# Optimization experiments

Measured on AMD Instinct MI355X. Metric: run time of the kernel, lower is better.

## Reference

```python
import jax, jax.numpy as jnp
import numpy as np
import math

CHUNK = 128  # hardcoded chunk_size in the original module


def setup_inputs() -> dict:
    key = jax.random.key(0)
    ks = jax.random.split(key, 6)
    B, C, T, H, W = 8, 256, 16, 8, 8
    KC, VC = 8192, 512  # key_channels, value_channels (dk = KC/heads = T*H*W = 1024)
    return {
        "x": jax.random.normal(ks[0], (B, C, T, H, W), dtype=jnp.float32),
        "Wk": jax.random.normal(ks[1], (KC, C), dtype=jnp.float32) * 0.02,
        "Wq": jax.random.normal(ks[2], (KC, C), dtype=jnp.float32) * 0.02,
        "Wv": jax.random.normal(ks[3], (VC, C), dtype=jnp.float32) * 0.02,
        "Wr": jax.random.normal(ks[4], (C, VC), dtype=jnp.float32) * 0.02,
        "br": jnp.zeros((C,), dtype=jnp.float32),
        "num_heads": 8,
    }


def reference(x, Wk, Wq, Wv, Wr, br, num_heads):
    B, C, T, H, W = x.shape
    N = T * H * W
    # 1x1x1 Conv3d == per-position linear projection
    k = jnp.einsum('oc,bcthw->bothw', Wk, x).reshape(B, num_heads, -1, N)
    q = jnp.einsum('oc,bcthw->bothw', Wq, x).reshape(B, num_heads, -1, N)
    v = jnp.einsum('oc,bcthw->bothw', Wv, x).reshape(B, num_heads, -1, N)
    dk = k.shape[2]  # == N by structural constraint of the original matmul
    # matmul(keys, q_chunk) over all chunks at once (matmul is linear in q):
    # contracts keys' position axis with queries' channel axis, as in torch.
    scores = jnp.matmul(k, q) / math.sqrt(dk)  # [B, h, dk, N]
    # softmax applied per query-chunk of size CHUNK along the last axis
    nchunks = N // CHUNK
    attn = jax.nn.softmax(
        scores.reshape(B, num_heads, dk, nchunks, CHUNK), axis=-1
    ).reshape(B, num_heads, dk, N)
    out = jnp.matmul(v, attn)  # [B, h, dv, N] (dk == N)
    out = out.reshape(B, -1, T, H, W)
    out = jnp.einsum('oc,bcthw->bothw', Wr, out) + br[None, :, None, None, None]
    return out
```

## Files before the change

### kernel.cpp

```cpp
#include <hip/hip_runtime.h>
#include <hip/hip_bf16.h>


using bf16x8 = __attribute__((ext_vector_type(8))) __bf16;
using f32x4  = __attribute__((ext_vector_type(4))) float;
using s16x4  = __attribute__((ext_vector_type(4))) short;

static __device__ __forceinline__ short f2b(float f) {
  union { float f; unsigned u; } v; v.f = f;
  unsigned r = v.u + 0x7fffu + ((v.u >> 16) & 1u);
  return (short)(r >> 16);
}

static __device__ __forceinline__ void gll16(const void* g, void* l) {
  __builtin_amdgcn_global_load_lds(
      (const __attribute__((address_space(1))) void*)g,
      (__attribute__((address_space(3))) void*)l, 16, 0, 0);
}

#define MFMA16(a, b, c) __builtin_amdgcn_mfma_f32_16x16x32_bf16((a), (b), (c), 0, 0, 0)

__global__ __launch_bounds__(256) void cvt_bf16(const float* __restrict__ in,
                                                short* __restrict__ out, int n) {
  int i = (blockIdx.x * 256 + threadIdx.x) * 4;
  if (i >= n) return;
  float4 v = *(const float4*)(in + i);
  s16x4 s = { f2b(v.x), f2b(v.y), f2b(v.z), f2b(v.w) };
  *(s16x4*)(out + i) = s;
}

__global__ __launch_bounds__(256) void tcvt(const float* __restrict__ in,
    short* __restrict__ outP, short* __restrict__ outT,
    int R, int C, long inB, long pB, long tB)
{
  __shared__ short tile[64][68];
  long bz = blockIdx.z;
  const float* src = in + bz * inB;
  int r0 = blockIdx.y * 64, c0 = blockIdx.x * 64;
  int t = threadIdx.x;
  int r = t >> 2, cq = (t & 3) * 16;
  #pragma unroll
  for (int e = 0; e < 16; e += 4) {
    float4 v = *(const float4*)(&src[(long)(r0 + r) * C + (c0 + cq + e)]);
    s16x4 s = { f2b(v.x), f2b(v.y), f2b(v.z), f2b(v.w) };
    *(s16x4*)(&tile[r][cq + e]) = s;
    if (outP) *(s16x4*)(&outP[bz * pB + (long)(r0 + r) * C + (c0 + cq + e)]) = s;
  }
  __syncthreads();
  int tr = t >> 2, re = (t & 3) * 16;
  short tmp[16];
  #pragma unroll
  for (int e = 0; e < 16; ++e) tmp[e] = tile[re + e][tr];
  short* dst = &outT[bz * tB + (long)(c0 + tr) * R + (r0 + re)];
  #pragma unroll
  for (int e = 0; e < 16; e += 4) *(s16x4*)(&dst[e]) = *(const s16x4*)(&tmp[e]);
}

template<bool F32OUT>
__global__ __launch_bounds__(256) void gemm_nt(
    const short* __restrict__ A, const short* __restrict__ B,
    void* __restrict__ C, const float* __restrict__ bias,
    int M, int N, int K, int lda, int ldb, int ldc,
    long aSB, long aSH, long bSB, long bSH, long cSB, long cSH, int nh)
{
  int batch = blockIdx.z;
  int hb = batch % nh, bb = batch / nh;
  const short* Ab = A + bb * aSB + hb * aSH;
  const short* Bb = B + bb * bSB + hb * bSH;
  long cOff = bb * cSB + hb * cSH;
  int m0 = blockIdx.y * 128, n0 = blockIdx.x * 128;
  __shared__ short As[128 * 64];
  __shared__ short Bs[128 * 64];
  int t = threadIdx.x;
  int lane = t & 63, wid = t >> 6;
  int wm = (wid >> 1) * 64, wn = (wid & 1) * 64;
  int rl = lane & 15, q = lane >> 4;
  f32x4 acc[4][4] = {};
  for (int k0 = 0; k0 < K; k0 += 64) {
    __syncthreads();
    #pragma unroll
    for (int j = 0; j < 4; ++j) {
      int g = j * 256 + t;
      int r = g >> 3, cc = g & 7;
      int cs = cc ^ (r & 7);
      gll16(&Ab[(long)(m0 + r) * lda + k0 + cs * 8], (char*)As + (j * 256 + wid * 64) * 16);
      gll16(&Bb[(long)(n0 + r) * ldb + k0 + cs * 8], (char*)Bs + (j * 256 + wid * 64) * 16);
    }
    __syncthreads();
    #pragma unroll
    for (int kt = 0; kt < 2; ++kt) {
      int cq = kt * 4 + q;
      bf16x8 af[4], bfv[4];
      #pragma unroll
      for (int mi = 0; mi < 4; ++mi) {
        int R = wm + 16 * mi + rl;
        af[mi] = *(const bf16x8*)((const char*)As + (R * 8 + (cq ^ (R & 7))) * 16);
      }
      #pragma unroll
      for (int ni = 0; ni < 4; ++ni) {
        int RN = wn + 16 * ni + rl;
        bfv[ni] = *(const bf16x8*)((const char*)Bs + (RN * 8 + (cq ^ (RN & 7))) * 16);
      }
      #pragma unroll
      for (int mi = 0; mi < 4; ++mi)
        #pragma unroll
        for (int ni = 0; ni < 4; ++ni)
          acc[mi][ni] = MFMA16(af[mi], bfv[ni], acc[mi][ni]);
    }
  }
  #pragma unroll
  for (int mi = 0; mi < 4; ++mi)
    #pragma unroll
    for (int ni = 0; ni < 4; ++ni)
      #pragma unroll
      for (int r = 0; r < 4; ++r) {
        int row = m0 + wm + 16 * mi + 4 * q + r;
        int col = n0 + wn + 16 * ni + rl;
        float val = acc[mi][ni][r];
        if (F32OUT) {
          ((float*)C)[cOff + (long)row * ldc + col] = val + (bias ? bias[row] : 0.f);
        } else {
          ((short*)C)[cOff + (long)row * ldc + col] = f2b(val);
        }
      }
}

__global__ __launch_bounds__(256, 2) void attn_fused(
    const short* __restrict__ Wk, const short* __restrict__ GT,
    const short* __restrict__ V, short* __restrict__ OT)
{
  __shared__ short smem[40960];
  short* As0 = smem;
  short* As1 = smem + 8192;
  short* Bs0 = smem + 16384;
  short* Bs1 = smem + 20480;
  short* aT  = smem + 24576;
  int blk = blockIdx.x;
  int c = blk & 7, h = (blk >> 3) & 7, b = blk >> 6;
  int t = threadIdx.x, lane = t & 63, w = t >> 6;
  int rl = lane & 15, q = lane >> 4;
  const short* Wkh = Wk + (long)(h * 1024) * 256;
  const short* GTc = GT + ((long)(b * 8 + h) * 1024 + c * 128) * 256;
  const short* Vb  = V + (long)(b * 512 + h * 64) * 1024;
  f32x4 ot[2][4] = {};
  const float SC = 1.4426950408889634f / 32.0f;

  auto stageA = [&](short* dst, int oRow, int k0) {
    #pragma unroll
    for (int j = 0; j < 4; ++j) {
      int g = j * 256 + t;
      int r = g >> 2, cc = g & 3;
      int cs = cc ^ ((r >> 1) & 3);
      gll16(&Wkh[(long)(oRow + r) * 256 + k0 + cs * 8],
            (char*)dst + (j * 256 + w * 64) * 16);
    }
  };
  auto stageB = [&](short* dst, int k0) {
    #pragma unroll
    for (int j = 0; j < 2; ++j) {
      int g = j * 256 + t;
      int r = g >> 2, cc = g & 3;
      int cs = cc ^ ((r >> 1) & 3);
      gll16(&GTc[(long)r * 256 + k0 + cs * 8],
            (char*)dst + (j * 256 + w * 64) * 16);
    }
  };

  short *Ac = As0, *An = As1, *Bc = Bs0, *Bn = Bs1;
  stageA(Ac, 0, 0);
  stageB(Bc, 0);
  __syncthreads();

  for (int o = 0; o < 4; ++o) {
    f32x4 s[4][8] = {};
    for (int sl = 0; sl < 8; ++sl) {
      int ns = sl + 1, no = o;
      if (ns == 8) { ns = 0; no = o + 1; }
      if (no < 4) { stageA(An, no * 256, ns * 32); stageB(Bn, ns * 32); }
      bf16x8 af[4];
      #pragma unroll
      for (int mi = 0; mi < 4; ++mi) {
        int R = w * 64 + 16 * mi + rl;
        af[mi] = *(const bf16x8*)((const char*)Ac + (R * 4 + (q ^ ((R >> 1) & 3))) * 16);
      }
      #pragma unroll
      for (int ni = 0; ni < 8; ++ni) {
        int Rj = 16 * ni + rl;
        bf16x8 bv = *(const bf16x8*)((const char*)Bc + (Rj * 4 + (q ^ ((Rj >> 1) & 3))) * 16);
        #pragma unroll
        for (int mi = 0; mi < 4; ++mi)
          s[mi][ni] = MFMA16(af[mi], bv, s[mi][ni]);
      }
      __syncthreads();
      short* tp;
      tp = Ac; Ac = An; An = tp;
      tp = Bc; Bc = Bn; Bn = tp;
    }
    float mx[4][4], sm[4][4], rc[4][4];
    #pragma unroll
    for (int mi = 0; mi < 4; ++mi)
      #pragma unroll
      for (int r = 0; r < 4; ++r) {
        float m = s[mi][0][r];
        #pragma unroll
        for (int ni = 1; ni < 8; ++ni) m = fmaxf(m, s[mi][ni][r]);
        mx[mi][r] = m;
      }
    #pragma unroll
    for (int msk = 1; msk < 16; msk <<= 1)
      #pragma unroll
      for (int mi = 0; mi < 4; ++mi)
        #pragma unroll
        for (int r = 0; r < 4; ++r)
          mx[mi][r] = fmaxf(mx[mi][r], __shfl_xor(mx[mi][r], msk, 64));
    #pragma unroll
    for (int mi = 0; mi < 4; ++mi)
      #pragma unroll
      for (int r = 0; r < 4; ++r) sm[mi][r] = 0.f;
    #pragma unroll
    for (int mi = 0; mi < 4; ++mi)
      #pragma unroll
      for (int ni = 0; ni < 8; ++ni)
        #pragma unroll
        for (int r = 0; r < 4; ++r) {
          float p = exp2f((s[mi][ni][r] - mx[mi][r]) * SC);
          s[mi][ni][r] = p;
          sm[mi][r] += p;
        }
    #pragma unroll
    for (int msk = 1; msk < 16; msk <<= 1)
      #pragma unroll
      for (int mi = 0; mi < 4; ++mi)
        #pragma unroll
        for (int r = 0; r < 4; ++r)
          sm[mi][r] += __shfl_xor(sm[mi][r], msk, 64);
    #pragma unroll
    for (int mi = 0; mi < 4; ++mi)
      #pragma unroll
      for (int r = 0; r < 4; ++r) rc[mi][r] = __builtin_amdgcn_rcpf(sm[mi][r]);

    #pragma unroll
    for (int hf = 0; hf < 2; ++hf) {
      if ((w >> 1) == hf) {
        #pragma unroll
        for (int mi = 0; mi < 4; ++mi)
          #pragma unroll
          for (int ni = 0; ni < 8; ++ni) {
            s16x4 pk = { f2b(s[mi][ni][0] * rc[mi][0]), f2b(s[mi][ni][1] * rc[mi][1]),
                         f2b(s[mi][ni][2] * rc[mi][2]), f2b(s[mi][ni][3] * rc[mi][3]) };
            int j  = 16 * ni + rl;
            int ci = (w & 1) * 8 + 2 * mi + (q >> 1);
            *(s16x4*)((char*)aT + j * 256 + (ci ^ (j & 7)) * 16 + (q & 1) * 8) = pk;
          }
      }
      __syncthreads();
      #pragma unroll
      for (int kt = 0; kt < 4; ++kt) {
        bf16x8 pa[2], vv[4];
        #pragma unroll
        for (int mi = 0; mi < 2; ++mi) {
          int Rj = 32 * w + 16 * mi + rl;
          int ci = kt * 4 + q;
          pa[mi] = *(const bf16x8*)((const char*)aT + Rj * 256 + (ci ^ (Rj & 7)) * 16);
        }
        int ig = o * 256 + hf * 128 + kt * 32 + q * 8;
        #pragma unroll
        for (int nd = 0; nd < 4; ++nd)
          vv[nd] = *(const bf16x8*)(&Vb[(long)(16 * nd + rl) * 1024 + ig]);
        #pragma unroll
        for (int mi = 0; mi < 2; ++mi)
          #pragma unroll
          for (int nd = 0; nd < 4; ++nd)
            ot[mi][nd] = MFMA16(pa[mi], vv[nd], ot[mi][nd]);
      }
      __syncthreads();
    }
  }
  short* OTb = OT + (long)(b * 1024 + c * 128) * 512 + h * 64;
  #pragma unroll
  for (int mi = 0; mi < 2; ++mi)
    #pragma unroll
    for (int nd = 0; nd < 4; ++nd)
      #pragma unroll
      for (int r = 0; r < 4; ++r) {
        int j = 32 * w + 16 * mi + 4 * q + r;
        int d = 16 * nd + rl;
        OTb[(long)j * 512 + d] = f2b(ot[mi][nd][r]);
      }
}

extern "C" void kernel_launch(void* const* d_in, const int* in_sizes, int n_in,
                              void* d_out, int out_size, void* d_ws, size_t ws_size,
                              hipStream_t stream)
{
  const float* x  = (const float*)d_in[0];
  const float* Wk = (const float*)d_in[1];
  const float* Wq = (const float*)d_in[2];
  const float* Wv = (const float*)d_in[3];
  const float* Wr = (const float*)d_in[4];
  const float* br = (const float*)d_in[5];
  float* out = (float*)d_out;

  char* ws = (char*)d_ws;
  short* Xbf = (short*)(ws + 0);
  short* XT  = (short*)(ws + 4194304);
  short* WqT = (short*)(ws + 8388608);
  short* Wkb = (short*)(ws + 12582912);
  short* Wvb = (short*)(ws + 16777216);
  short* Wrb = (short*)(ws + 17039360);
  short* Mb  = (short*)(ws + 17301504);
  short* GTb = (short*)(ws + 25690112);
  short* Vbf = (short*)(ws + 59244544);
  short* OTb = (short*)(ws + 67633152);

  tcvt<<<dim3(16, 4, 8), 256, 0, stream>>>(x, Xbf, XT, 256, 1024, 262144L, 262144L, 262144L);
  tcvt<<<dim3(4, 128, 1), 256, 0, stream>>>(Wq, nullptr, WqT, 8192, 256, 0L, 0L, 0L);
  cvt_bf16<<<2048, 256, 0, stream>>>(Wk, Wkb, 2097152);
  cvt_bf16<<<128, 256, 0, stream>>>(Wv, Wvb, 131072);
  cvt_bf16<<<128, 256, 0, stream>>>(Wr, Wrb, 131072);

  gemm_nt<false><<<dim3(2, 2, 64), 256, 0, stream>>>(Xbf, WqT, Mb, nullptr,
      256, 256, 1024, 1024, 8192, 256,
      262144L, 0L, 0L, 1024L, 524288L, 65536L, 8);
  gemm_nt<false><<<dim3(2, 8, 64), 256, 0, stream>>>(XT, Mb, GTb, nullptr,
      1024, 256, 256, 256, 256, 256,
      262144L, 0L, 524288L, 65536L, 2097152L, 262144L, 8);
  gemm_nt<false><<<dim3(8, 4, 8), 256, 0, stream>>>(Wvb, XT, Vbf, nullptr,
      512, 1024, 256, 256, 256, 1024,
      0L, 0L, 262144L, 0L, 524288L, 0L, 1);
  attn_fused<<<512, 256, 0, stream>>>(Wkb, GTb, Vbf, OTb);
  gemm_nt<true><<<dim3(8, 2, 8), 256, 0, stream>>>(Wrb, OTb, out, br,
      256, 1024, 512, 512, 512, 1024,
      0L, 0L, 524288L, 0L, 262144L, 0L, 1);
}
```

Baseline: 295.8 us.

## Split fused attention into score-softmax and PV kernels via materialized attention

Replaces the single fused attention kernel (512 blocks, each doing QK, chunked softmax and PV serially over four row groups) with two kernels. The first computes 128x128 score tiles, applies the softmax and writes normalized bf16 probabilities to a workspace buffer. The second multiplies those probabilities by V. Work is processed in batch slices sized to the available workspace, which raises the block count per launch at the cost of extra global traffic for the attention matrix and several more launches.

```diff
diff --git a/kernel.cpp b/kernel.cpp
--- a/kernel.cpp
+++ b/kernel.cpp
@@ -125,168 +125,164 @@
       }
 }
 
-__global__ __launch_bounds__(256, 2) void attn_fused(
+__global__ __launch_bounds__(256) void qk_soft(
     const short* __restrict__ Wk, const short* __restrict__ GT,
-    const short* __restrict__ V, short* __restrict__ OT)
-{
-  __shared__ short smem[40960];
-  short* As0 = smem;
-  short* As1 = smem + 8192;
-  short* Bs0 = smem + 16384;
-  short* Bs1 = smem + 20480;
-  short* aT  = smem + 24576;
-  int blk = blockIdx.x;
-  int c = blk & 7, h = (blk >> 3) & 7, b = blk >> 6;
+    short* __restrict__ attnT)
+{
+  __shared__ short smem[16384];
+  short* As = smem;
+  short* Bs = smem + 8192;
+  int c = blockIdx.x, it = blockIdx.y, z = blockIdx.z;
+  int h = z & 7;
   int t = threadIdx.x, lane = t & 63, w = t >> 6;
   int rl = lane & 15, q = lane >> 4;
-  const short* Wkh = Wk + (long)(h * 1024) * 256;
-  const short* GTc = GT + ((long)(b * 8 + h) * 1024 + c * 128) * 256;
-  const short* Vb  = V + (long)(b * 512 + h * 64) * 1024;
-  f32x4 ot[2][4] = {};
+  const short* Ab = Wk + (long)(h * 1024 + it * 128) * 256;
+  const short* Bb = GT + ((long)z * 1024 + c * 128) * 256;
   const float SC = 1.4426950408889634f / 32.0f;
-
-  auto stageA = [&](short* dst, int oRow, int k0) {
+  f32x4 s[2][8] = {};
+  for (int k0 = 0; k0 < 256; k0 += 64) {
+    __syncthreads();
     #pragma unroll
     for (int j = 0; j < 4; ++j) {
       int g = j * 256 + t;
-      int r = g >> 2, cc = g & 3;
-      int cs = cc ^ ((r >> 1) & 3);
-      gll16(&Wkh[(long)(oRow + r) * 256 + k0 + cs * 8],
-            (char*)dst + (j * 256 + w * 64) * 16);
-    }
-  };
-  auto stageB = [&](short* dst, int k0) {
+      int r = g >> 3, cc = g & 7, cs = cc ^ (r & 7);
+      gll16(&Ab[(long)r * 256 + k0 + cs * 8], (char*)As + (j * 256 + w * 64) * 16);
+      gll16(&Bb[(long)r * 256 + k0 + cs * 8], (char*)Bs + (j * 256 + w * 64) * 16);
+    }
+    __syncthreads();
+    #pragma unroll
+    for (int kt = 0; kt < 2; ++kt) {
+      int cq = kt * 4 + q;
+      bf16x8 af[2];
+      #pragma unroll
+      for (int mi = 0; mi < 2; ++mi) {
+        int R = 32 * w + 16 * mi + rl;
+        af[mi] = *(const bf16x8*)((const char*)As + (R * 8 + (cq ^ (R & 7))) * 16);
+      }
+      #pragma unroll
+      for (int ni = 0; ni < 8; ++ni) {
+        int RN = 16 * ni + rl;
+        bf16x8 bv = *(const bf16x8*)((const char*)Bs + (RN * 8 + (cq ^ (RN & 7))) * 16);
+        #pragma unroll
+        for (int mi = 0; mi < 2; ++mi)
+          s[mi][ni] = MFMA16(af[mi], bv, s[mi][ni]);
+      }
+    }
+  }
+  __syncthreads();
+  float mx[2][4], sm[2][4], rc[2][4];
+  #pragma unroll
+  for (int mi = 0; mi < 2; ++mi)
+    #pragma unroll
+    for (int r = 0; r < 4; ++r) {
+      float m = s[mi][0][r];
+      #pragma unroll
+      for (int ni = 1; ni < 8; ++ni) m = fmaxf(m, s[mi][ni][r]);
+      mx[mi][r] = m;
+    }
+  #pragma unroll
+  for (int msk = 1; msk < 16; msk <<= 1)
+    #pragma unroll
+    for (int mi = 0; mi < 2; ++mi)
+      #pragma unroll
+      for (int r = 0; r < 4; ++r)
+        mx[mi][r] = fmaxf(mx[mi][r], __shfl_xor(mx[mi][r], msk, 64));
+  #pragma unroll
+  for (int mi = 0; mi < 2; ++mi)
+    #pragma unroll
+    for (int r = 0; r < 4; ++r) sm[mi][r] = 0.f;
+  #pragma unroll
+  for (int mi = 0; mi < 2; ++mi)
+    #pragma unroll
+    for (int ni = 0; ni < 8; ++ni)
+      #pragma unroll
+      for (int r = 0; r < 4; ++r) {
+        float p = exp2f((s[mi][ni][r] - mx[mi][r]) * SC);
+        s[mi][ni][r] = p;
+        sm[mi][r] += p;
+      }
+  #pragma unroll
+  for (int msk = 1; msk < 16; msk <<= 1)
+    #pragma unroll
+    for (int mi = 0; mi < 2; ++mi)
+      #pragma unroll
+      for (int r = 0; r < 4; ++r)
+        sm[mi][r] += __shfl_xor(sm[mi][r], msk, 64);
+  #pragma unroll
+  for (int mi = 0; mi < 2; ++mi)
+    #pragma unroll
+    for (int r = 0; r < 4; ++r) rc[mi][r] = __builtin_amdgcn_rcpf(sm[mi][r]);
+  #pragma unroll
+  for (int mi = 0; mi < 2; ++mi)
+    #pragma unroll
+    for (int ni = 0; ni < 8; ++ni) {
+      s16x4 pk = { f2b(s[mi][ni][0] * rc[mi][0]), f2b(s[mi][ni][1] * rc[mi][1]),
+                   f2b(s[mi][ni][2] * rc[mi][2]), f2b(s[mi][ni][3] * rc[mi][3]) };
+      int j  = 16 * ni + rl;
+      int ci = 4 * w + 2 * mi + (q >> 1);
+      *(s16x4*)((char*)smem + j * 256 + ((ci ^ (j & 7)) * 16) + (q & 1) * 8) = pk;
+    }
+  __syncthreads();
+  int j = t >> 1, half = t & 1;
+  long base = ((long)z * 1024 + c * 128 + j) * 1024 + it * 128 + half * 64;
+  #pragma unroll
+  for (int e = 0; e < 8; ++e) {
+    int ch = half * 8 + e;
+    int4 v = *(const int4*)((const char*)smem + j * 256 + (ch ^ (j & 7)) * 16);
+    *(int4*)(&attnT[base + e * 8]) = v;
+  }
+}
+
+__global__ __launch_bounds__(256) void pv(
+    const short* __restrict__ attnT, const short* __restrict__ V,
+    short* __restrict__ OT)
+{
+  __shared__ short smem[6144];
+  short* As = smem;
+  short* Bs = smem + 2048;
+  int jt = blockIdx.x, z = blockIdx.z;
+  int bl = z >> 3, h = z & 7;
+  int t = threadIdx.x, lane = t & 63, w = t >> 6;
+  int rl = lane & 15, q = lane >> 4;
+  int wj = (w >> 1) * 16, wd = (w & 1) * 32;
+  const short* Ab = attnT + ((long)z * 1024 + jt * 32) * 1024;
+  const short* Bb = V + (long)(bl * 512 + h * 64) * 1024;
+  short* Ob = OT + (long)(bl * 1024 + jt * 32) * 512 + h * 64;
+  f32x4 acc[2] = {};
+  for (int k0 = 0; k0 < 1024; k0 += 64) {
+    __syncthreads();
+    {
+      int r = t >> 3, cc = t & 7, cs = cc ^ (r & 7);
+      gll16(&Ab[(long)r * 1024 + k0 + cs * 8], (char*)As + (w * 64) * 16);
+    }
     #pragma unroll
     for (int j = 0; j < 2; ++j) {
       int g = j * 256 + t;
-      int r = g >> 2, cc = g & 3;
-      int cs = cc ^ ((r >> 1) & 3);
-      gll16(&GTc[(long)r * 256 + k0 + cs * 8],
-            (char*)dst + (j * 256 + w * 64) * 16);
-    }
-  };
-
-  short *Ac = As0, *An = As1, *Bc = Bs0, *Bn = Bs1;
-  stageA(Ac, 0, 0);
-  stageB(Bc, 0);
-  __syncthreads();
-
-  for (int o = 0; o < 4; ++o) {
-    f32x4 s[4][8] = {};
-    for (int sl = 0; sl < 8; ++sl) {
-      int ns = sl + 1, no = o;
-      if (ns == 8) { ns = 0; no = o + 1; }
-      if (no < 4) { stageA(An, no * 256, ns * 32); stageB(Bn, ns * 32); }
-      bf16x8 af[4];
-      #pragma unroll
-      for (int mi = 0; mi < 4; ++mi) {
-        int R = w * 64 + 16 * mi + rl;
-        af[mi] = *(const bf16x8*)((const char*)Ac + (R * 4 + (q ^ ((R >> 1) & 3))) * 16);
-      }
-      #pragma unroll
-      for (int ni = 0; ni < 8; ++ni) {
-        int Rj = 16 * ni + rl;
-        bf16x8 bv = *(const bf16x8*)((const char*)Bc + (Rj * 4 + (q ^ ((Rj >> 1) & 3))) * 16);
-        #pragma unroll
-        for (int mi = 0; mi < 4; ++mi)
-          s[mi][ni] = MFMA16(af[mi], bv, s[mi][ni]);
-      }
-      __syncthreads();
-      short* tp;
-      tp = Ac; Ac = An; An = tp;
-      tp = Bc; Bc = Bn; Bn = tp;
-    }
-    float mx[4][4], sm[4][4], rc[4][4];
-    #pragma unroll
-    for (int mi = 0; mi < 4; ++mi)
-      #pragma unroll
-      for (int r = 0; r < 4; ++r) {
-        float m = s[mi][0][r];
-        #pragma unroll
-        for (int ni = 1; ni < 8; ++ni) m = fmaxf(m, s[mi][ni][r]);
-        mx[mi][r] = m;
-      }
-    #pragma unroll
-    for (int msk = 1; msk < 16; msk <<= 1)
-      #pragma unroll
-      for (int mi = 0; mi < 4; ++mi)
-        #pragma unroll
-        for (int r = 0; r < 4; ++r)
-          mx[mi][r] = fmaxf(mx[mi][r], __shfl_xor(mx[mi][r], msk, 64));
-    #pragma unroll
-    for (int mi = 0; mi < 4; ++mi)
-      #pragma unroll
-      for (int r = 0; r < 4; ++r) sm[mi][r] = 0.f;
-    #pragma unroll
-    for (int mi = 0; mi < 4; ++mi)
-      #pragma unroll
-      for (int ni = 0; ni < 8; ++ni)
-        #pragma unroll
-        for (int r = 0; r < 4; ++r) {
-          float p = exp2f((s[mi][ni][r] - mx[mi][r]) * SC);
-          s[mi][ni][r] = p;
-          sm[mi][r] += p;
-        }
-    #pragma unroll
-    for (int msk = 1; msk < 16; msk <<= 1)
-      #pragma unroll
-      for (int mi = 0; mi < 4; ++mi)
-        #pragma unroll
-        for (int r = 0; r < 4; ++r)
-          sm[mi][r] += __shfl_xor(sm[mi][r], msk, 64);
-    #pragma unroll
-    for (int mi = 0; mi < 4; ++mi)
-      #pragma unroll
-      for (int r = 0; r < 4; ++r) rc[mi][r] = __builtin_amdgcn_rcpf(sm[mi][r]);
-
-    #pragma unroll
-    for (int hf = 0; hf < 2; ++hf) {
-      if ((w >> 1) == hf) {
-        #pragma unroll
-        for (int mi = 0; mi < 4; ++mi)
-          #pragma unroll
-          for (int ni = 0; ni < 8; ++ni) {
-            s16x4 pk = { f2b(s[mi][ni][0] * rc[mi][0]), f2b(s[mi][ni][1] * rc[mi][1]),
-                         f2b(s[mi][ni][2] * rc[mi][2]), f2b(s[mi][ni][3] * rc[mi][3]) };
-            int j  = 16 * ni + rl;
-            int ci = (w & 1) * 8 + 2 * mi + (q >> 1);
-            *(s16x4*)((char*)aT + j * 256 + (ci ^ (j & 7)) * 16 + (q & 1) * 8) = pk;
-          }
-      }
-      __syncthreads();
-      #pragma unroll
-      for (int kt = 0; kt < 4; ++kt) {
-        bf16x8 pa[2], vv[4];
-        #pragma unroll
-        for (int mi = 0; mi < 2; ++mi) {
-          int Rj = 32 * w + 16 * mi + rl;
-          int ci = kt * 4 + q;
-          pa[mi] = *(const bf16x8*)((const char*)aT + Rj * 256 + (ci ^ (Rj & 7)) * 16);
-        }
-        int ig = o * 256 + hf * 128 + kt * 32 + q * 8;
-        #pragma unroll
-        for (int nd = 0; nd < 4; ++nd)
-          vv[nd] = *(const bf16x8*)(&Vb[(long)(16 * nd + rl) * 1024 + ig]);
-        #pragma unroll
-        for (int mi = 0; mi < 2; ++mi)
-          #pragma unroll
-          for (int nd = 0; nd < 4; ++nd)
-            ot[mi][nd] = MFMA16(pa[mi], vv[nd], ot[mi][nd]);
-      }
-      __syncthreads();
-    }
-  }
-  short* OTb = OT + (long)(b * 1024 + c * 128) * 512 + h * 64;
-  #pragma unroll
-  for (int mi = 0; mi < 2; ++mi)
-    #pragma unroll
-    for (int nd = 0; nd < 4; ++nd)
-      #pragma unroll
-      for (int r = 0; r < 4; ++r) {
-        int j = 32 * w + 16 * mi + 4 * q + r;
-        int d = 16 * nd + rl;
-        OTb[(long)j * 512 + d] = f2b(ot[mi][nd][r]);
-      }
+      int r = g >> 3, cc = g & 7, cs = cc ^ (r & 7);
+      gll16(&Bb[(long)r * 1024 + k0 + cs * 8], (char*)Bs + (j * 256 + w * 64) * 16);
+    }
+    __syncthreads();
+    #pragma unroll
+    for (int kt = 0; kt < 2; ++kt) {
+      int cq = kt * 4 + q;
+      int R = wj + rl;
+      bf16x8 af = *(const bf16x8*)((const char*)As + (R * 8 + (cq ^ (R & 7))) * 16);
+      #pragma unroll
+      for (int nd = 0; nd < 2; ++nd) {
+        int RN = wd + 16 * nd + rl;
+        bf16x8 bv = *(const bf16x8*)((const char*)Bs + (RN * 8 + (cq ^ (RN & 7))) * 16);
+        acc[nd] = MFMA16(af, bv, acc[nd]);
+      }
+    }
+  }
+  #pragma unroll
+  for (int nd = 0; nd < 2; ++nd)
+    #pragma unroll
+    for (int r = 0; r < 4; ++r) {
+      int jl = wj + 4 * q + r;
+      int d  = wd + 16 * nd + rl;
+      Ob[(long)jl * 512 + d] = f2b(acc[nd][r]);
+    }
 }
 
 extern "C" void kernel_launch(void* const* d_in, const int* in_sizes, int n_in,
@@ -313,6 +309,11 @@
   short* Vbf = (short*)(ws + 59244544);
   short* OTb = (short*)(ws + 67633152);
 
+  bool big = ws_size >= (size_t)110000000;
+  short* attnT = big ? (short*)(ws + 76021760) : (short*)ws;
+  int NB = big ? 4 : 8;
+  int NZ = big ? 16 : 8;
+
   tcvt<<<dim3(16, 4, 8), 256, 0, stream>>>(x, Xbf, XT, 256, 1024, 262144L, 262144L, 262144L);
   tcvt<<<dim3(4, 128, 1), 256, 0, stream>>>(Wq, nullptr, WqT, 8192, 256, 0L, 0L, 0L);
   cvt_bf16<<<2048, 256, 0, stream>>>(Wk, Wkb, 2097152);
@@ -328,7 +329,14 @@
   gemm_nt<false><<<dim3(8, 4, 8), 256, 0, stream>>>(Wvb, XT, Vbf, nullptr,
       512, 1024, 256, 256, 256, 1024,
       0L, 0L, 262144L, 0L, 524288L, 0L, 1);
-  attn_fused<<<512, 256, 0, stream>>>(Wkb, GTb, Vbf, OTb);
+
+  for (int bb = 0; bb < NB; ++bb) {
+    qk_soft<<<dim3(8, 8, NZ), 256, 0, stream>>>(
+        Wkb, GTb + (long)bb * NZ * 262144, attnT);
+    pv<<<dim3(32, 1, NZ), 256, 0, stream>>>(
+        attnT, Vbf + (long)bb * NZ * 65536, OTb + (long)bb * NZ * 65536);
+  }
+
   gemm_nt<true><<<dim3(8, 2, 8), 256, 0, stream>>>(Wrb, OTb, out, br,
       256, 1024, 512, 512, 512, 1024,
       0L, 0L, 524288L, 0L, 262144L, 0L, 1);
```

After: 332.9 us. 12.5% more time.
